# Optimization experiments

Measured on AMD Instinct MI355X. Metric: run time of the kernel, lower is better.

The kernel has to match this reference:

```python
import jax, jax.numpy as jnp
import numpy as np

N = 50000
E = 800000
IN_DIM = 256
HID_DIM = 256
OUT_DIM = 128


def _gcn(x, src, dst, W, b):
    # PyG GCNConv: h = W x; add self-loops; sym-normalized scatter-add; + bias
    h = x @ W  # [N, out]
    deg = jax.ops.segment_sum(jnp.ones_like(dst, dtype=h.dtype), dst, num_segments=N)
    dinv = jax.lax.rsqrt(jnp.maximum(deg, 1e-12))
    norm = dinv[src] * dinv[dst]  # [E+N]
    msg = h[src] * norm[:, None]  # gather + scale
    out = jax.ops.segment_sum(msg, dst, num_segments=N)  # scatter-add
    return out + b


def _with_self_loops(edge):
    loops = jnp.arange(N, dtype=edge.dtype)
    src = jnp.concatenate([edge[0], loops])
    dst = jnp.concatenate([edge[1], loops])
    return src, dst


def setup_inputs() -> dict:
    key = jax.random.key(0)
    ks = jax.random.split(key, 20)
    d = {}
    d['x'] = jax.random.normal(ks[0], (N, IN_DIM), dtype=jnp.float32)
    d['edge_ppi'] = jax.random.randint(ks[1], (2, E), 0, N, dtype=jnp.int32)
    d['edge_path'] = jax.random.randint(ks[2], (2, E), 0, N, dtype=jnp.int32)
    d['edge_go'] = jax.random.randint(ks[3], (2, E), 0, N, dtype=jnp.int32)
    i = 4
    for name in ['ppi', 'path', 'go']:
        s1 = 1.0 / np.sqrt(IN_DIM)
        s2 = 1.0 / np.sqrt(HID_DIM)
        d[f'{name}_w1'] = jax.random.uniform(ks[i], (IN_DIM, HID_DIM), jnp.float32, -s1, s1); i += 1
        d[f'{name}_b1'] = jnp.zeros((HID_DIM,), jnp.float32)
        d[f'{name}_w2'] = jax.random.uniform(ks[i], (HID_DIM, OUT_DIM), jnp.float32, -s2, s2); i += 1
        d[f'{name}_b2'] = jnp.zeros((OUT_DIM,), jnp.float32)
    sa = 1.0 / np.sqrt(OUT_DIM)
    d['attn_w'] = jax.random.uniform(ks[i], (OUT_DIM, 1), jnp.float32, -sa, sa)
    d['attn_b'] = jnp.zeros((1,), jnp.float32)
    return d


def reference(x, edge_ppi, edge_path, edge_go,
              ppi_w1, ppi_b1, ppi_w2, ppi_b2,
              path_w1, path_b1, path_w2, path_b2,
              go_w1, go_b1, go_w2, go_b2,
              attn_w, attn_b):
    feats = []
    for edge, w1, b1, w2, b2 in [
        (edge_ppi, ppi_w1, ppi_b1, ppi_w2, ppi_b2),
        (edge_path, path_w1, path_b1, path_w2, path_b2),
        (edge_go, go_w1, go_b1, go_w2, go_b2),
    ]:
        src, dst = _with_self_loops(edge)
        h = jax.nn.relu(_gcn(x, src, dst, w1, b1))
        feats.append(_gcn(h, src, dst, w2, b2))
    all_feat = jnp.stack(feats, axis=1)  # [N, 3, out]
    attn = jax.nn.softmax(all_feat @ attn_w + attn_b, axis=1)  # [N, 3, 1]
    return jnp.sum(all_feat * attn, axis=1)  # [N, out]
```

## Files before the change

kernel.cpp:

```cpp
#include <hip/hip_runtime.h>

#define NN 50000
#define NE 800000
#define BINS 98
#define CAP 12288
#define EPB 4096
#define P1B ((NE + EPB - 1) / EPB)

typedef __attribute__((ext_vector_type(8))) short short8;
typedef __attribute__((ext_vector_type(4))) float f32x4;
typedef __attribute__((ext_vector_type(8))) unsigned short ushort8v;
typedef __attribute__((ext_vector_type(4))) unsigned short ushort4v;
typedef _Float16 half8 __attribute__((ext_vector_type(8)));

__device__ __forceinline__ ushort f2bf(float f) {
    unsigned u = __float_as_uint(f);
    unsigned r = (u + 0x7fffu + ((u >> 16) & 1u)) >> 16;
    return (ushort)r;
}
__device__ __forceinline__ float bf2f(ushort h) {
    return __uint_as_float(((unsigned)h) << 16);
}
__device__ __forceinline__ ushort f2h(float f) {
    _Float16 h = (_Float16)f;
    return __builtin_bit_cast(ushort, h);
}
__device__ __forceinline__ float h2f(ushort u) {
    return (float)__builtin_bit_cast(_Float16, u);
}


__global__ __launch_bounds__(256) void k_bin(const int* __restrict__ e0,
                                             const int* __restrict__ e1,
                                             const int* __restrict__ e2,
                                             int* __restrict__ g_cur,
                                             unsigned* __restrict__ g_bins) {
    const int br = blockIdx.x / P1B;
    const int cb = blockIdx.x % P1B;
    const int* ep = (br == 0 ? e0 : br == 1 ? e1 : e2);
    const int tid = threadIdx.x;
    const int e_base = cb * EPB;

    __shared__ int s_cnt[BINS];
    __shared__ int s_start[BINS];
    __shared__ int s_cur[BINS];
    __shared__ int s_gb[BINS];
    __shared__ unsigned s_stage[EPB];

    if (tid < BINS) s_cnt[tid] = 0;
    __syncthreads();

    int4 s4[4], d4[4];
    bool valid[4];
#pragma unroll
    for (int i = 0; i < 4; ++i) {
        int idx = e_base + i * 1024 + tid * 4;
        valid[i] = (idx < NE);
        if (valid[i]) {
            s4[i] = *(const int4*)&ep[idx];
            d4[i] = *(const int4*)&ep[NE + idx];
            atomicAdd(&s_cnt[d4[i].x >> 9], 1);
            atomicAdd(&s_cnt[d4[i].y >> 9], 1);
            atomicAdd(&s_cnt[d4[i].z >> 9], 1);
            atomicAdd(&s_cnt[d4[i].w >> 9], 1);
        }
    }
    __syncthreads();
    if (tid == 0) {
        int run = 0;
        for (int b = 0; b < BINS; ++b) {
            s_start[b] = run;
            run += s_cnt[b];
        }
    }
    __syncthreads();
    if (tid < BINS) {
        s_cur[tid] = s_start[tid];
        int c = s_cnt[tid];
        int pc = (c + 15) & ~15;
        s_gb[tid] = (c > 0) ? atomicAdd(&g_cur[br * BINS + tid], pc) : 0;
    }
    __syncthreads();

#pragma unroll
    for (int i = 0; i < 4; ++i) {
        if (valid[i]) {
            int ss[4] = {s4[i].x, s4[i].y, s4[i].z, s4[i].w};
            int dd[4] = {d4[i].x, d4[i].y, d4[i].z, d4[i].w};
#pragma unroll
            for (int q = 0; q < 4; ++q) {
                int bin = dd[q] >> 9;
                int pos = atomicAdd(&s_cur[bin], 1);
                s_stage[pos] = ((unsigned)(dd[q] & 511) << 16) | (unsigned)ss[q];
            }
        }
    }
    __syncthreads();

    for (int b = 0; b < BINS; ++b) {
        int c = s_cnt[b];
        if (c == 0) continue;
        int st = s_start[b];
        int gb = s_gb[b];
        int pc = (c + 15) & ~15;
        if (gb + pc > CAP) pc = (gb < CAP) ? (CAP - gb) : 0;
        size_t obase = (size_t)(br * BINS + b) * CAP + gb;
        for (int j = tid; j < pc; j += 256)
            g_bins[obase + j] = (j < c) ? s_stage[st + j] : 0x80000000u;
    }
}


__device__ __forceinline__ int wave_incl_scan(int v, int lane) {
#pragma unroll
    for (int d = 1; d < 64; d <<= 1) {
        int u = __shfl_up(v, d);
        if (lane >= d) v += u;
    }
    return v;
}

__global__ __launch_bounds__(256) void k_build(const unsigned* __restrict__ g_bins,
                                               const int* __restrict__ g_cur,
                                               ushort* __restrict__ g_csr,
                                               int* __restrict__ seg3,
                                               int* __restrict__ cnt3,
                                               float* __restrict__ dinv3) {
    const int bid = blockIdx.x;
    const int br = bid / BINS;
    const int b2 = bid % BINS;
    const size_t base = (size_t)bid * CAP;
    const int node0 = b2 << 9;
    const int tid = threadIdx.x;

    __shared__ int s_cnt[512];
    __shared__ int s_off[512];
    __shared__ int s_wsum[4];

    s_cnt[tid] = 0;
    s_cnt[tid + 256] = 0;
    __syncthreads();

    const int total = min(g_cur[bid], CAP);
    for (int j = tid; j < total; j += 256) {
        unsigned p = g_bins[base + j];
        if (!(p & 0x80000000u)) atomicAdd(&s_cnt[(p >> 16) & 0x1FF], 1);
    }
    __syncthreads();

    const int lane = tid & 63, w = tid >> 6;
    int c0 = s_cnt[2 * tid], c1 = s_cnt[2 * tid + 1];
    int c2 = c0 + c1;
    int incl = wave_incl_scan(c2, lane);
    if (lane == 63) s_wsum[w] = incl;
    __syncthreads();
    int wpre = 0;
    for (int i = 0; i < w; ++i) wpre += s_wsum[i];
    int ex = wpre + incl - c2;
    s_off[2 * tid] = ex;
    s_off[2 * tid + 1] = ex + c0;

#pragma unroll
    for (int q = 0; q < 2; ++q) {
        int local = 2 * tid + q;
        int node = node0 + local;
        if (node < NN) {
            int g = br * NN + node;
            int c = (q == 0) ? c0 : c1;
            seg3[g] = (int)base + s_off[local];
            cnt3[g] = c;
            dinv3[g] = rsqrtf((float)(c + 1));
        }
    }
    __syncthreads();
    s_cnt[2 * tid] = s_off[2 * tid];
    s_cnt[2 * tid + 1] = s_off[2 * tid + 1];
    __syncthreads();

    for (int j = tid; j < total; j += 256) {
        unsigned p = g_bins[base + j];
        if (!(p & 0x80000000u)) {
            int loc = (p >> 16) & 0x1FF;
            int pos = atomicAdd(&s_cnt[loc], 1);
            g_csr[base + pos] = (ushort)(p & 0xFFFFu);
        }
    }
}


__global__ __launch_bounds__(256) void k_conv_x(const float* __restrict__ x,
                                                ushort* __restrict__ xp) {
    const int wid = threadIdx.x >> 6, lane = threadIdx.x & 63;
    const int row = blockIdx.x * 4 + wid;
    if (row >= NN) return;
    float4 v = *(const float4*)&x[(size_t)row * 256 + lane * 4];
    ushort4 hi, lo;
    hi.x = f2bf(v.x); lo.x = f2bf(v.x - bf2f(hi.x));
    hi.y = f2bf(v.y); lo.y = f2bf(v.y - bf2f(hi.y));
    hi.z = f2bf(v.z); lo.z = f2bf(v.z - bf2f(hi.z));
    hi.w = f2bf(v.w); lo.w = f2bf(v.w - bf2f(hi.w));
    *(ushort4*)&xp[(size_t)row * 512 + lane * 4] = hi;
    *(ushort4*)&xp[(size_t)row * 512 + 256 + lane * 4] = lo;
}

__global__ __launch_bounds__(256) void k_conv_w1(const float* __restrict__ w0,
                                                 const float* __restrict__ w1,
                                                 const float* __restrict__ w2,
                                                 ushort* __restrict__ BT1all) {
    int idx = blockIdx.x * 256 + threadIdx.x;
    int b = idx >> 16, r = idx & 65535;
    int k = r >> 8, n = r & 255;
    const float* W = (b == 0 ? w0 : b == 1 ? w1 : w2);
    float w = W[r];
    ushort hi = f2bf(w);
    ushort lo = f2bf(w - bf2f(hi));
    ushort* row = BT1all + (size_t)b * 196608 + (size_t)n * 768;
    row[k] = hi;
    row[256 + k] = hi;
    row[512 + k] = lo;
}

__global__ __launch_bounds__(256) void k_conv_w2(const float* __restrict__ w0,
                                                 const float* __restrict__ w1,
                                                 const float* __restrict__ w2,
                                                 ushort* __restrict__ BT2all) {
    int idx = blockIdx.x * 256 + threadIdx.x;
    int b = idx >> 15, r = idx & 32767;
    int k = r >> 7, n = r & 127;
    const float* W = (b == 0 ? w0 : b == 1 ? w1 : w2);
    BT2all[(size_t)b * 32768 + (size_t)n * 256 + k] = f2h(W[r]);
}


template <int BM, int BN, int N, int KK, int AK, bool HALF, bool XSWZ>
__global__ __launch_bounds__((BM / 64) * (BN / 64) * 64) void k_gemm(
    const ushort* __restrict__ A, size_t aBatch,
    const ushort* __restrict__ BTall, int btBatch,
    const float* __restrict__ dinv3, ushort* __restrict__ Call, size_t cBatch) {
    constexpr int WGN = BN / 64, NW = (BM / 64) * WGN;
    constexpr int BK = 32;
    constexpr int MT = (NN + BM - 1) / BM, NT = N / BN, GB = MT * NT;
    constexpr int NSTEP = KK / BK;
    __shared__ ushort sA[2][BM * BK];
    __shared__ ushort sB[2][BN * BK];
    int kb, bid;
    if constexpr (XSWZ) {
        int q = blockIdx.x >> 3, r = blockIdx.x & 7;
        bid = (q / 3) * 8 + r;
        kb = q % 3;
        if (bid >= GB) return;
    } else {
        kb = blockIdx.x / GB;
        bid = blockIdx.x % GB;
    }
    const ushort* Ab = A + (size_t)kb * aBatch;
    const ushort* BT = BTall + (size_t)kb * btBatch;
    const float* dinv = dinv3 + (size_t)kb * NN;
    ushort* C = Call + (size_t)kb * cBatch;
    const int t = threadIdx.x, lane = t & 63, wid = t >> 6;
    const int wm = (wid / WGN) * 64, wn = (wid % WGN) * 64;
    const int bm = (bid / NT) * BM;
    const int bn = (bid % NT) * BN;

    f32x4 zero = {0.f, 0.f, 0.f, 0.f};
    f32x4 acc[4][4];
#pragma unroll
    for (int m = 0; m < 4; ++m)
#pragma unroll
        for (int n = 0; n < 4; ++n) acc[m][n] = zero;

    constexpr int A_ISS = (BM * BK * 2) / (NW * 1024);
    constexpr int B_ISS = (BN * BK * 2) / (NW * 1024);

    auto stage = [&](int buf, int kt) {
        const int akt = (kt >= AK) ? kt - AK : kt;
#pragma unroll
        for (int i = 0; i < A_ISS; ++i) {
            int off = (wid + i * NW) << 10;
            int la = off + lane * 16;
            int row = la >> 6;
            int slot = (la >> 4) & 3;
            int scol = (slot ^ (row & 3)) << 4;
            int grow = bm + row;
            if (grow > NN - 1) grow = NN - 1;
            const char* ga = (const char*)Ab + (size_t)grow * (AK * 2) + akt * 2 + scol;
            __builtin_amdgcn_global_load_lds(
                (__attribute__((address_space(1))) const void*)ga,
                (__attribute__((address_space(3))) void*)((char*)sA[buf] + off), 16, 0, 0);
        }
#pragma unroll
        for (int i = 0; i < B_ISS; ++i) {
            int off = (wid + i * NW) << 10;
            int la = off + lane * 16;
            int row = la >> 6;
            int slot = (la >> 4) & 3;
            int scol = (slot ^ (row & 3)) << 4;
            const char* ga = (const char*)BT + (size_t)(bn + row) * (KK * 2) + kt * 2 + scol;
            __builtin_amdgcn_global_load_lds(
                (__attribute__((address_space(1))) const void*)ga,
                (__attribute__((address_space(3))) void*)((char*)sB[buf] + off), 16, 0, 0);
        }
    };

    stage(0, 0);
    __syncthreads();

    int cur = 0;
    for (int ts = 0; ts < NSTEP; ++ts) {
        if (ts + 1 < NSTEP) stage(cur ^ 1, (ts + 1) * BK);

        const int s = lane >> 4;
        const int r0 = lane & 15;
        short8 af[4], bf[4];
#pragma unroll
        for (int m = 0; m < 4; ++m) {
            int row = wm + m * 16 + r0;
            af[m] = *(const short8*)((const char*)sA[cur] + row * 64 + ((s ^ (row & 3)) << 4));
        }
#pragma unroll
        for (int n = 0; n < 4; ++n) {
            int row = wn + n * 16 + r0;
            bf[n] = *(const short8*)((const char*)sB[cur] + row * 64 + ((s ^ (row & 3)) << 4));
        }
#pragma unroll
        for (int m = 0; m < 4; ++m)
#pragma unroll
            for (int n = 0; n < 4; ++n) {
                if constexpr (HALF)
                    acc[m][n] = __builtin_amdgcn_mfma_f32_16x16x32_f16(
                        __builtin_bit_cast(half8, af[m]), __builtin_bit_cast(half8, bf[n]),
                        acc[m][n], 0, 0, 0);
                else
                    acc[m][n] = __builtin_amdgcn_mfma_f32_16x16x32_bf16(af[m], bf[n],
                                                                        acc[m][n], 0, 0, 0);
            }
        __syncthreads();
        cur ^= 1;
    }

    const int cr0 = (lane >> 4) * 4;
    const int cc = lane & 15;
#pragma unroll
    for (int m = 0; m < 4; ++m) {
#pragma unroll
        for (int r = 0; r < 4; ++r) {
            int row = bm + wm + m * 16 + cr0 + r;
            if (row < NN) {
                float dv = dinv[row];
#pragma unroll
                for (int n = 0; n < 4; ++n)
                    C[(size_t)row * N + bn + wn + n * 16 + cc] = f2h(acc[m][n][r] * dv);
            }
        }
    }
}


#define UTOT (3 * 12500)

__global__ __launch_bounds__(256) void k_agg1(const ushort* __restrict__ hs16all,
                                              const int* __restrict__ seg3,
                                              const int* __restrict__ cnt3,
                                              const ushort* __restrict__ g_csr,
                                              const float* __restrict__ dinv3,
                                              const float* __restrict__ b1a,
                                              const float* __restrict__ b1b,
                                              const float* __restrict__ b1c,
                                              ushort* __restrict__ h1all) {
    const int x = blockIdx.x & 7, j = blockIdx.x >> 3;
    const int start = (x * UTOT) >> 3;
    const int end = ((x + 1) * UTOT) >> 3;
    const int u = start + j;
    if (u >= end) return;
    const int b = u / 12500;
    const int blk = u % 12500;

    const int wid = threadIdx.x >> 6;
    const int lane = threadIdx.x & 63;
    const int node = blk * 4 + wid;
    if (node >= NN) return;
    const int half = lane >> 5, l32 = lane & 31;
    const int g = b * NN + node;
    const ushort* hs = hs16all + (size_t)b * NN * 256;
    const ushort* csr = g_csr + seg3[g];
    const int len = cnt3[g] + 1;
    const size_t colb = (size_t)l32 * 8;

    float acc[8] = {0.f, 0.f, 0.f, 0.f, 0.f, 0.f, 0.f, 0.f};
    int i = half;
    for (; i + 6 < len; i += 8) {
        int s0 = (i == 0) ? node : (int)csr[i - 1];
        int s1 = (int)csr[i + 1];
        int s2 = (int)csr[i + 3];
        int s3 = (int)csr[i + 5];
        ushort8v v0 = *(const ushort8v*)&hs[(size_t)s0 * 256 + colb];
        ushort8v v1 = *(const ushort8v*)&hs[(size_t)s1 * 256 + colb];
        ushort8v v2 = *(const ushort8v*)&hs[(size_t)s2 * 256 + colb];
        ushort8v v3 = *(const ushort8v*)&hs[(size_t)s3 * 256 + colb];
#pragma unroll
        for (int jq = 0; jq < 8; ++jq)
            acc[jq] += (h2f(v0[jq]) + h2f(v1[jq])) + (h2f(v2[jq]) + h2f(v3[jq]));
    }
    for (; i < len; i += 2) {
        int s = (i == 0) ? node : (int)csr[i - 1];
        ushort8v v = *(const ushort8v*)&hs[(size_t)s * 256 + colb];
#pragma unroll
        for (int jq = 0; jq < 8; ++jq) acc[jq] += h2f(v[jq]);
    }
#pragma unroll
    for (int jq = 0; jq < 8; ++jq) acc[jq] += __shfl_xor(acc[jq], 32);

    if (half == 0) {
        const float* bias = (b == 0 ? b1a : b == 1 ? b1b : b1c);
        const float di = dinv3[g];
        ushort8v o;
#pragma unroll
        for (int jq = 0; jq < 8; ++jq) {
            float r = fmaxf(di * acc[jq] + bias[l32 * 8 + jq], 0.f);
            o[jq] = f2h(r);
        }
        *(ushort8v*)&h1all[((size_t)b * NN + node) * 256 + colb] = o;
    }
}


__global__ __launch_bounds__(256) void k_final(const ushort* __restrict__ hs2all,
                                               const int* __restrict__ seg3,
                                               const int* __restrict__ cnt3,
                                               const ushort* __restrict__ g_csr,
                                               const float* __restrict__ dinv3,
                                               const float* __restrict__ b2a,
                                               const float* __restrict__ b2b,
                                               const float* __restrict__ b2c,
                                               const float* __restrict__ attn_w,
                                               const float* __restrict__ attn_b,
                                               float* __restrict__ out) {
    const int wid = threadIdx.x >> 6;
    const int lane = threadIdx.x & 63;
    const int node = blockIdx.x * 4 + wid;
    if (node >= NN) return;
    const int half = lane >> 5, l32 = lane & 31;
    const size_t colb = (size_t)l32 * 4;

    float f[3][4];
#pragma unroll
    for (int b = 0; b < 3; ++b) {
        const int g = b * NN + node;
        const ushort* hs = hs2all + (size_t)b * NN * 128;
        const ushort* csr = g_csr + seg3[g];
        const int len = cnt3[g] + 1;
        float acc[4] = {0.f, 0.f, 0.f, 0.f};
        int i = half;
        for (; i + 6 < len; i += 8) {
            int s0 = (i == 0) ? node : (int)csr[i - 1];
            int s1 = (int)csr[i + 1];
            int s2 = (int)csr[i + 3];
            int s3 = (int)csr[i + 5];
            ushort4v v0 = *(const ushort4v*)&hs[(size_t)s0 * 128 + colb];
            ushort4v v1 = *(const ushort4v*)&hs[(size_t)s1 * 128 + colb];
            ushort4v v2 = *(const ushort4v*)&hs[(size_t)s2 * 128 + colb];
            ushort4v v3 = *(const ushort4v*)&hs[(size_t)s3 * 128 + colb];
#pragma unroll
            for (int j = 0; j < 4; ++j)
                acc[j] += (h2f(v0[j]) + h2f(v1[j])) + (h2f(v2[j]) + h2f(v3[j]));
        }
        for (; i < len; i += 2) {
            int s = (i == 0) ? node : (int)csr[i - 1];
            ushort4v v = *(const ushort4v*)&hs[(size_t)s * 128 + colb];
#pragma unroll
            for (int j = 0; j < 4; ++j) acc[j] += h2f(v[j]);
        }
#pragma unroll
        for (int j = 0; j < 4; ++j) acc[j] += __shfl_xor(acc[j], 32);
        const float* bias = (b == 0 ? b2a : b == 1 ? b2b : b2c);
        const float di = dinv3[g];
#pragma unroll
        for (int j = 0; j < 4; ++j) f[b][j] = di * acc[j] + bias[l32 * 4 + j];
    }

    float4 w = *(const float4*)&attn_w[l32 * 4];
    float s0 = f[0][0] * w.x + f[0][1] * w.y + f[0][2] * w.z + f[0][3] * w.w;
    float s1 = f[1][0] * w.x + f[1][1] * w.y + f[1][2] * w.z + f[1][3] * w.w;
    float s2 = f[2][0] * w.x + f[2][1] * w.y + f[2][2] * w.z + f[2][3] * w.w;
#pragma unroll
    for (int m = 16; m >= 1; m >>= 1) {
        s0 += __shfl_xor(s0, m);
        s1 += __shfl_xor(s1, m);
        s2 += __shfl_xor(s2, m);
    }
    float bb = attn_b[0];
    s0 += bb; s1 += bb; s2 += bb;
    float mx = fmaxf(s0, fmaxf(s1, s2));
    float e0 = expf(s0 - mx), e1 = expf(s1 - mx), e2 = expf(s2 - mx);
    float inv = 1.f / (e0 + e1 + e2);
    e0 *= inv; e1 *= inv; e2 *= inv;

    if (half == 0) {
        float4 o;
        o.x = f[0][0] * e0 + f[1][0] * e1 + f[2][0] * e2;
        o.y = f[0][1] * e0 + f[1][1] * e1 + f[2][1] * e2;
        o.z = f[0][2] * e0 + f[1][2] * e1 + f[2][2] * e2;
        o.w = f[0][3] * e0 + f[1][3] * e1 + f[2][3] * e2;
        *(float4*)&out[(size_t)node * 128 + colb] = o;
    }
}


extern "C" void kernel_launch(void* const* d_in, const int* in_sizes, int n_in,
                              void* d_out, int out_size, void* d_ws, size_t ws_size,
                              hipStream_t stream) {
    const float* x = (const float*)d_in[0];
    const int* e0 = (const int*)d_in[1];
    const int* e1 = (const int*)d_in[2];
    const int* e2 = (const int*)d_in[3];
    const float* attn_w = (const float*)d_in[16];
    const float* attn_b = (const float*)d_in[17];

    char* ws = (char*)d_ws;
    size_t off = 0;
    auto alloc = [&](size_t bytes) -> void* {
        void* p = ws + off;
        off += (bytes + 255) & ~(size_t)255;
        return p;
    };

    int* g_cur      = (int*)alloc(3 * BINS * 4);
    int* seg3       = (int*)alloc((size_t)3 * NN * 4);
    int* cnt3       = (int*)alloc((size_t)3 * NN * 4);
    float* dinv3    = (float*)alloc((size_t)3 * NN * 4);
    ushort* g_csr   = (ushort*)alloc((size_t)3 * BINS * CAP * 2);
    ushort* xp      = (ushort*)alloc((size_t)NN * 512 * 2);
    ushort* hs2all  = xp;
    ushort* hs16all = (ushort*)alloc((size_t)3 * NN * 256 * 2);
    ushort* h1all   = (ushort*)alloc((size_t)3 * NN * 256 * 2);
    unsigned* g_bins = (unsigned*)h1all;
    ushort* BT1all  = (ushort*)alloc((size_t)3 * 256 * 768 * 2);
    ushort* BT2all  = (ushort*)alloc((size_t)3 * 128 * 256 * 2);

    const int WB = (NN + 3) / 4;

    hipMemsetAsync(g_cur, 0, 3 * BINS * 4, stream);
    k_conv_x<<<WB, 256, 0, stream>>>(x, xp);
    k_conv_w1<<<768, 256, 0, stream>>>((const float*)d_in[4], (const float*)d_in[8],
                                       (const float*)d_in[12], BT1all);
    k_conv_w2<<<384, 256, 0, stream>>>((const float*)d_in[6], (const float*)d_in[10],
                                       (const float*)d_in[14], BT2all);

    k_bin<<<3 * P1B, 256, 0, stream>>>(e0, e1, e2, g_cur, g_bins);
    k_build<<<3 * BINS, 256, 0, stream>>>(g_bins, g_cur, g_csr, seg3, cnt3, dinv3);

    k_gemm<128, 256, 256, 768, 512, false, true><<<1176, 512, 0, stream>>>(
        xp, 0, BT1all, 196608, dinv3, hs16all, (size_t)NN * 256);
    k_agg1<<<8 * ((UTOT + 7) / 8), 256, 0, stream>>>(
        hs16all, seg3, cnt3, g_csr, dinv3,
        (const float*)d_in[5], (const float*)d_in[9], (const float*)d_in[13], h1all);

    k_gemm<128, 128, 128, 256, 256, true, false><<<3 * 391, 256, 0, stream>>>(
        h1all, (size_t)NN * 256, BT2all, 32768, dinv3, hs2all, (size_t)NN * 128);

    k_final<<<WB, 256, 0, stream>>>(hs2all, seg3, cnt3, g_csr, dinv3,
                                    (const float*)d_in[7], (const float*)d_in[11],
                                    (const float*)d_in[15], attn_w, attn_b,
                                    (float*)d_out);
}
```

Baseline: 475.6 us.

## Partition sparse aggregation by column slices over node chunks; split final into feat+attn

The two aggregation kernels are restructured so that each wave owns a 32-column slice of one branch and walks a chunk of 32 consecutive nodes, gathering a single fp16 element per lane rather than a full row segment. Column groups are spread across the 8 XCD-interleaved block slots, so each XCD's L2 only has to cache a column slice of the gathered feature matrix, which is meant to improve cache reuse. The final stage is split into a per-branch aggregation that writes fp16 features to scratch, followed by a separate attention-softmax kernel. In exchange, the gathers become narrow 2-byte loads, the feature values pass through an extra fp16 round-trip, and one more launch is added.

```diff
diff --git a/kernel.cpp b/kernel.cpp
--- a/kernel.cpp
+++ b/kernel.cpp
@@ -7,10 +7,15 @@
 #define EPB 4096
 #define P1B ((NE + EPB - 1) / EPB)
 
+#define CH 1563
+#define CLS1 24
+#define T1 (CLS1 * CH)
+#define TPX1 (T1 / 8)
+#define CLS2 12
+#define T2 (CLS2 * CH)
+
 typedef __attribute__((ext_vector_type(8))) short short8;
 typedef __attribute__((ext_vector_type(4))) float f32x4;
-typedef __attribute__((ext_vector_type(8))) unsigned short ushort8v;
-typedef __attribute__((ext_vector_type(4))) unsigned short ushort4v;
 typedef _Float16 half8 __attribute__((ext_vector_type(8)));
 
 __device__ __forceinline__ ushort f2bf(float f) {
@@ -356,8 +361,6 @@
 }
 
 
-#define UTOT (3 * 12500)
-
 __global__ __launch_bounds__(256) void k_agg1(const ushort* __restrict__ hs16all,
                                               const int* __restrict__ seg3,
                                               const int* __restrict__ cnt3,
@@ -367,123 +370,127 @@
                                               const float* __restrict__ b1b,
                                               const float* __restrict__ b1c,
                                               ushort* __restrict__ h1all) {
-    const int x = blockIdx.x & 7, j = blockIdx.x >> 3;
-    const int start = (x * UTOT) >> 3;
-    const int end = ((x + 1) * UTOT) >> 3;
-    const int u = start + j;
-    if (u >= end) return;
-    const int b = u / 12500;
-    const int blk = u % 12500;
-
-    const int wid = threadIdx.x >> 6;
-    const int lane = threadIdx.x & 63;
-    const int node = blk * 4 + wid;
-    if (node >= NN) return;
+    const int x = blockIdx.x & 7, jb = blockIdx.x >> 3;
+    const int w = threadIdx.x >> 6, lane = threadIdx.x & 63;
+    const int tj = jb * 4 + w;
+    if (tj >= TPX1) return;
+    const int t = x * TPX1 + tj;
+    const int cls = t / CH, chunk = t % CH;
+    const int br = cls >> 3, cg = cls & 7;
     const int half = lane >> 5, l32 = lane & 31;
-    const int g = b * NN + node;
-    const ushort* hs = hs16all + (size_t)b * NN * 256;
-    const ushort* csr = g_csr + seg3[g];
-    const int len = cnt3[g] + 1;
-    const size_t colb = (size_t)l32 * 8;
-
-    float acc[8] = {0.f, 0.f, 0.f, 0.f, 0.f, 0.f, 0.f, 0.f};
-    int i = half;
-    for (; i + 6 < len; i += 8) {
-        int s0 = (i == 0) ? node : (int)csr[i - 1];
-        int s1 = (int)csr[i + 1];
-        int s2 = (int)csr[i + 3];
-        int s3 = (int)csr[i + 5];
-        ushort8v v0 = *(const ushort8v*)&hs[(size_t)s0 * 256 + colb];
-        ushort8v v1 = *(const ushort8v*)&hs[(size_t)s1 * 256 + colb];
-        ushort8v v2 = *(const ushort8v*)&hs[(size_t)s2 * 256 + colb];
-        ushort8v v3 = *(const ushort8v*)&hs[(size_t)s3 * 256 + colb];
-#pragma unroll
-        for (int jq = 0; jq < 8; ++jq)
-            acc[jq] += (h2f(v0[jq]) + h2f(v1[jq])) + (h2f(v2[jq]) + h2f(v3[jq]));
-    }
-    for (; i < len; i += 2) {
-        int s = (i == 0) ? node : (int)csr[i - 1];
-        ushort8v v = *(const ushort8v*)&hs[(size_t)s * 256 + colb];
-#pragma unroll
-        for (int jq = 0; jq < 8; ++jq) acc[jq] += h2f(v[jq]);
-    }
-#pragma unroll
-    for (int jq = 0; jq < 8; ++jq) acc[jq] += __shfl_xor(acc[jq], 32);
-
-    if (half == 0) {
-        const float* bias = (b == 0 ? b1a : b == 1 ? b1b : b1c);
-        const float di = dinv3[g];
-        ushort8v o;
-#pragma unroll
-        for (int jq = 0; jq < 8; ++jq) {
-            float r = fmaxf(di * acc[jq] + bias[l32 * 8 + jq], 0.f);
-            o[jq] = f2h(r);
-        }
-        *(ushort8v*)&h1all[((size_t)b * NN + node) * 256 + colb] = o;
-    }
-}
-
-
-__global__ __launch_bounds__(256) void k_final(const ushort* __restrict__ hs2all,
-                                               const int* __restrict__ seg3,
-                                               const int* __restrict__ cnt3,
-                                               const ushort* __restrict__ g_csr,
-                                               const float* __restrict__ dinv3,
-                                               const float* __restrict__ b2a,
-                                               const float* __restrict__ b2b,
-                                               const float* __restrict__ b2c,
-                                               const float* __restrict__ attn_w,
-                                               const float* __restrict__ attn_b,
-                                               float* __restrict__ out) {
-    const int wid = threadIdx.x >> 6;
-    const int lane = threadIdx.x & 63;
-    const int node = blockIdx.x * 4 + wid;
-    if (node >= NN) return;
-    const int half = lane >> 5, l32 = lane & 31;
-    const size_t colb = (size_t)l32 * 4;
-
-    float f[3][4];
-#pragma unroll
-    for (int b = 0; b < 3; ++b) {
-        const int g = b * NN + node;
-        const ushort* hs = hs2all + (size_t)b * NN * 128;
+    const int col = cg * 32 + l32;
+    const ushort* hs = hs16all + (size_t)br * NN * 256 + col;
+    const float* bias = (br == 0 ? b1a : br == 1 ? b1b : b1c);
+    const float bcol = bias[col];
+    const int n1 = min(chunk * 32 + 32, NN);
+
+    for (int node = chunk * 32; node < n1; ++node) {
+        const int g = br * NN + node;
         const ushort* csr = g_csr + seg3[g];
         const int len = cnt3[g] + 1;
-        float acc[4] = {0.f, 0.f, 0.f, 0.f};
+        float acc = 0.f;
         int i = half;
         for (; i + 6 < len; i += 8) {
             int s0 = (i == 0) ? node : (int)csr[i - 1];
             int s1 = (int)csr[i + 1];
             int s2 = (int)csr[i + 3];
             int s3 = (int)csr[i + 5];
-            ushort4v v0 = *(const ushort4v*)&hs[(size_t)s0 * 128 + colb];
-            ushort4v v1 = *(const ushort4v*)&hs[(size_t)s1 * 128 + colb];
-            ushort4v v2 = *(const ushort4v*)&hs[(size_t)s2 * 128 + colb];
-            ushort4v v3 = *(const ushort4v*)&hs[(size_t)s3 * 128 + colb];
-#pragma unroll
-            for (int j = 0; j < 4; ++j)
-                acc[j] += (h2f(v0[j]) + h2f(v1[j])) + (h2f(v2[j]) + h2f(v3[j]));
+            float v0 = h2f(hs[(size_t)s0 * 256]);
+            float v1 = h2f(hs[(size_t)s1 * 256]);
+            float v2 = h2f(hs[(size_t)s2 * 256]);
+            float v3 = h2f(hs[(size_t)s3 * 256]);
+            acc += (v0 + v1) + (v2 + v3);
         }
         for (; i < len; i += 2) {
             int s = (i == 0) ? node : (int)csr[i - 1];
-            ushort4v v = *(const ushort4v*)&hs[(size_t)s * 128 + colb];
-#pragma unroll
-            for (int j = 0; j < 4; ++j) acc[j] += h2f(v[j]);
-        }
-#pragma unroll
-        for (int j = 0; j < 4; ++j) acc[j] += __shfl_xor(acc[j], 32);
-        const float* bias = (b == 0 ? b2a : b == 1 ? b2b : b2c);
-        const float di = dinv3[g];
-#pragma unroll
-        for (int j = 0; j < 4; ++j) f[b][j] = di * acc[j] + bias[l32 * 4 + j];
-    }
-
-    float4 w = *(const float4*)&attn_w[l32 * 4];
-    float s0 = f[0][0] * w.x + f[0][1] * w.y + f[0][2] * w.z + f[0][3] * w.w;
-    float s1 = f[1][0] * w.x + f[1][1] * w.y + f[1][2] * w.z + f[1][3] * w.w;
-    float s2 = f[2][0] * w.x + f[2][1] * w.y + f[2][2] * w.z + f[2][3] * w.w;
-#pragma unroll
-    for (int m = 16; m >= 1; m >>= 1) {
+            acc += h2f(hs[(size_t)s * 256]);
+        }
+        acc += __shfl_xor(acc, 32);
+        if (half == 0) {
+            float r = fmaxf(dinv3[g] * acc + bcol, 0.f);
+            h1all[(size_t)g * 256 + col] = f2h(r);
+        }
+    }
+}
+
+
+__global__ __launch_bounds__(256) void k_feat(const ushort* __restrict__ hs2all,
+                                              const int* __restrict__ seg3,
+                                              const int* __restrict__ cnt3,
+                                              const ushort* __restrict__ g_csr,
+                                              const float* __restrict__ dinv3,
+                                              const float* __restrict__ b2a,
+                                              const float* __restrict__ b2b,
+                                              const float* __restrict__ b2c,
+                                              ushort* __restrict__ feats) {
+    const int x = blockIdx.x & 7, jb = blockIdx.x >> 3;
+    const int w = threadIdx.x >> 6, lane = threadIdx.x & 63;
+    const int start = (x * T2) >> 3;
+    const int end = ((x + 1) * T2) >> 3;
+    const int t = start + jb * 4 + w;
+    if (t >= end) return;
+    const int cls = t / CH, chunk = t % CH;
+    const int br = cls >> 2, cg = cls & 3;
+    const int half = lane >> 5, l32 = lane & 31;
+    const int col = cg * 32 + l32;
+    const ushort* hs = hs2all + (size_t)br * NN * 128 + col;
+    const float* bias = (br == 0 ? b2a : br == 1 ? b2b : b2c);
+    const float bcol = bias[col];
+    const int n1 = min(chunk * 32 + 32, NN);
+
+    for (int node = chunk * 32; node < n1; ++node) {
+        const int g = br * NN + node;
+        const ushort* csr = g_csr + seg3[g];
+        const int len = cnt3[g] + 1;
+        float acc = 0.f;
+        int i = half;
+        for (; i + 6 < len; i += 8) {
+            int s0 = (i == 0) ? node : (int)csr[i - 1];
+            int s1 = (int)csr[i + 1];
+            int s2 = (int)csr[i + 3];
+            int s3 = (int)csr[i + 5];
+            float v0 = h2f(hs[(size_t)s0 * 128]);
+            float v1 = h2f(hs[(size_t)s1 * 128]);
+            float v2 = h2f(hs[(size_t)s2 * 128]);
+            float v3 = h2f(hs[(size_t)s3 * 128]);
+            acc += (v0 + v1) + (v2 + v3);
+        }
+        for (; i < len; i += 2) {
+            int s = (i == 0) ? node : (int)csr[i - 1];
+            acc += h2f(hs[(size_t)s * 128]);
+        }
+        acc += __shfl_xor(acc, 32);
+        if (half == 0) {
+            float f = dinv3[g] * acc + bcol;
+            feats[(size_t)node * 384 + br * 128 + col] = f2h(f);
+        }
+    }
+}
+
+
+__global__ __launch_bounds__(256) void k_attn(const ushort* __restrict__ feats,
+                                              const float* __restrict__ attn_w,
+                                              const float* __restrict__ attn_b,
+                                              float* __restrict__ out) {
+    const int wid = threadIdx.x >> 6;
+    const int lane = threadIdx.x & 63;
+    const int node = blockIdx.x * 4 + wid;
+    if (node >= NN) return;
+
+    float2 w = *(const float2*)&attn_w[lane * 2];
+    const ushort* f = feats + (size_t)node * 384;
+    ushort2 u0 = *(const ushort2*)&f[0 * 128 + lane * 2];
+    ushort2 u1 = *(const ushort2*)&f[1 * 128 + lane * 2];
+    ushort2 u2 = *(const ushort2*)&f[2 * 128 + lane * 2];
+    float f0x = h2f(u0.x), f0y = h2f(u0.y);
+    float f1x = h2f(u1.x), f1y = h2f(u1.y);
+    float f2x = h2f(u2.x), f2y = h2f(u2.y);
+
+    float s0 = f0x * w.x + f0y * w.y;
+    float s1 = f1x * w.x + f1y * w.y;
+    float s2 = f2x * w.x + f2y * w.y;
+#pragma unroll
+    for (int m = 32; m >= 1; m >>= 1) {
         s0 += __shfl_xor(s0, m);
         s1 += __shfl_xor(s1, m);
         s2 += __shfl_xor(s2, m);
@@ -495,14 +502,10 @@
     float inv = 1.f / (e0 + e1 + e2);
     e0 *= inv; e1 *= inv; e2 *= inv;
 
-    if (half == 0) {
-        float4 o;
-        o.x = f[0][0] * e0 + f[1][0] * e1 + f[2][0] * e2;
-        o.y = f[0][1] * e0 + f[1][1] * e1 + f[2][1] * e2;
-        o.z = f[0][2] * e0 + f[1][2] * e1 + f[2][2] * e2;
-        o.w = f[0][3] * e0 + f[1][3] * e1 + f[2][3] * e2;
-        *(float4*)&out[(size_t)node * 128 + colb] = o;
-    }
+    float2 o;
+    o.x = f0x * e0 + f1x * e1 + f2x * e2;
+    o.y = f0y * e0 + f1y * e1 + f2y * e2;
+    *(float2*)&out[(size_t)node * 128 + lane * 2] = o;
 }
 
 
@@ -534,6 +537,7 @@
     ushort* hs16all = (ushort*)alloc((size_t)3 * NN * 256 * 2);
     ushort* h1all   = (ushort*)alloc((size_t)3 * NN * 256 * 2);
     unsigned* g_bins = (unsigned*)h1all;
+    ushort* feats   = h1all;
     ushort* BT1all  = (ushort*)alloc((size_t)3 * 256 * 768 * 2);
     ushort* BT2all  = (ushort*)alloc((size_t)3 * 128 * 256 * 2);
 
@@ -551,15 +555,15 @@
 
     k_gemm<128, 256, 256, 768, 512, false, true><<<1176, 512, 0, stream>>>(
         xp, 0, BT1all, 196608, dinv3, hs16all, (size_t)NN * 256);
-    k_agg1<<<8 * ((UTOT + 7) / 8), 256, 0, stream>>>(
+    k_agg1<<<8 * ((TPX1 + 3) / 4), 256, 0, stream>>>(
         hs16all, seg3, cnt3, g_csr, dinv3,
         (const float*)d_in[5], (const float*)d_in[9], (const float*)d_in[13], h1all);
 
     k_gemm<128, 128, 128, 256, 256, true, false><<<3 * 391, 256, 0, stream>>>(
         h1all, (size_t)NN * 256, BT2all, 32768, dinv3, hs2all, (size_t)NN * 128);
 
-    k_final<<<WB, 256, 0, stream>>>(hs2all, seg3, cnt3, g_csr, dinv3,
-                                    (const float*)d_in[7], (const float*)d_in[11],
-                                    (const float*)d_in[15], attn_w, attn_b,
-                                    (float*)d_out);
-}
+    k_feat<<<8 * ((((T2 + 7) / 8) + 3) / 4), 256, 0, stream>>>(
+        hs2all, seg3, cnt3, g_csr, dinv3,
+        (const float*)d_in[7], (const float*)d_in[11], (const float*)d_in[15], feats);
+    k_attn<<<WB, 256, 0, stream>>>(feats, attn_w, attn_b, (float*)d_out);
+}
```

New measurement: 1.028 ms. +116.1%, slower.

## Fuse layer-1 aggregation with layer-2 GEMM through shared-memory tile

Applied to the files above, without the earlier changes.

Merges the first-layer neighbor aggregation and the second-layer weight GEMM into one kernel. Each block aggregates 16 nodes into a swizzled LDS tile, then multiplies it by W2 with MFMA and writes hs2 directly. This drops the h1 intermediate round-trip to global memory and one kernel launch. In exchange, W2 is reloaded from global or L2 by every block, the output stores are narrow 2-byte writes, and the XCD-aware block remapping the old aggregation kernel used is gone.

```diff
diff --git a/kernel.cpp b/kernel.cpp
--- a/kernel.cpp
+++ b/kernel.cpp
@@ -356,70 +356,97 @@
 }
 
 
-#define UTOT (3 * 12500)
-
-__global__ __launch_bounds__(256) void k_agg1(const ushort* __restrict__ hs16all,
-                                              const int* __restrict__ seg3,
-                                              const int* __restrict__ cnt3,
-                                              const ushort* __restrict__ g_csr,
-                                              const float* __restrict__ dinv3,
-                                              const float* __restrict__ b1a,
-                                              const float* __restrict__ b1b,
-                                              const float* __restrict__ b1c,
-                                              ushort* __restrict__ h1all) {
-    const int x = blockIdx.x & 7, j = blockIdx.x >> 3;
-    const int start = (x * UTOT) >> 3;
-    const int end = ((x + 1) * UTOT) >> 3;
-    const int u = start + j;
-    if (u >= end) return;
-    const int b = u / 12500;
-    const int blk = u % 12500;
-
-    const int wid = threadIdx.x >> 6;
-    const int lane = threadIdx.x & 63;
-    const int node = blk * 4 + wid;
-    if (node >= NN) return;
+__global__ __launch_bounds__(256) void k_agg1g2(
+    const ushort* __restrict__ hs16all, const int* __restrict__ seg3,
+    const int* __restrict__ cnt3, const ushort* __restrict__ g_csr,
+    const float* __restrict__ dinv3,
+    const float* __restrict__ b1a, const float* __restrict__ b1b,
+    const float* __restrict__ b1c,
+    const ushort* __restrict__ BT2all, ushort* __restrict__ hs2all) {
+    const int br = blockIdx.x / 3125;
+    const int blk = blockIdx.x % 3125;
+    const int node0 = blk * 16;
+    const int w = threadIdx.x >> 6, lane = threadIdx.x & 63;
     const int half = lane >> 5, l32 = lane & 31;
-    const int g = b * NN + node;
-    const ushort* hs = hs16all + (size_t)b * NN * 256;
-    const ushort* csr = g_csr + seg3[g];
-    const int len = cnt3[g] + 1;
+
+    __shared__ ushort h1s[16 * 256];
+
+    const ushort* hs = hs16all + (size_t)br * NN * 256;
+    const float* bias = (br == 0 ? b1a : br == 1 ? b1b : b1c);
     const size_t colb = (size_t)l32 * 8;
 
-    float acc[8] = {0.f, 0.f, 0.f, 0.f, 0.f, 0.f, 0.f, 0.f};
-    int i = half;
-    for (; i + 6 < len; i += 8) {
-        int s0 = (i == 0) ? node : (int)csr[i - 1];
-        int s1 = (int)csr[i + 1];
-        int s2 = (int)csr[i + 3];
-        int s3 = (int)csr[i + 5];
-        ushort8v v0 = *(const ushort8v*)&hs[(size_t)s0 * 256 + colb];
-        ushort8v v1 = *(const ushort8v*)&hs[(size_t)s1 * 256 + colb];
-        ushort8v v2 = *(const ushort8v*)&hs[(size_t)s2 * 256 + colb];
-        ushort8v v3 = *(const ushort8v*)&hs[(size_t)s3 * 256 + colb];
-#pragma unroll
-        for (int jq = 0; jq < 8; ++jq)
-            acc[jq] += (h2f(v0[jq]) + h2f(v1[jq])) + (h2f(v2[jq]) + h2f(v3[jq]));
-    }
-    for (; i < len; i += 2) {
-        int s = (i == 0) ? node : (int)csr[i - 1];
-        ushort8v v = *(const ushort8v*)&hs[(size_t)s * 256 + colb];
-#pragma unroll
-        for (int jq = 0; jq < 8; ++jq) acc[jq] += h2f(v[jq]);
-    }
-#pragma unroll
-    for (int jq = 0; jq < 8; ++jq) acc[jq] += __shfl_xor(acc[jq], 32);
-
-    if (half == 0) {
-        const float* bias = (b == 0 ? b1a : b == 1 ? b1b : b1c);
-        const float di = dinv3[g];
-        ushort8v o;
-#pragma unroll
-        for (int jq = 0; jq < 8; ++jq) {
-            float r = fmaxf(di * acc[jq] + bias[l32 * 8 + jq], 0.f);
-            o[jq] = f2h(r);
-        }
-        *(ushort8v*)&h1all[((size_t)b * NN + node) * 256 + colb] = o;
+#pragma unroll 1
+    for (int q = 0; q < 4; ++q) {
+        const int r = w * 4 + q;
+        const int node = node0 + r;
+        const int g = br * NN + node;
+        const ushort* csr = g_csr + seg3[g];
+        const int len = cnt3[g] + 1;
+
+        float acc[8] = {0.f, 0.f, 0.f, 0.f, 0.f, 0.f, 0.f, 0.f};
+        int i = half;
+        for (; i + 6 < len; i += 8) {
+            int s0 = (i == 0) ? node : (int)csr[i - 1];
+            int s1 = (int)csr[i + 1];
+            int s2 = (int)csr[i + 3];
+            int s3 = (int)csr[i + 5];
+            ushort8v v0 = *(const ushort8v*)&hs[(size_t)s0 * 256 + colb];
+            ushort8v v1 = *(const ushort8v*)&hs[(size_t)s1 * 256 + colb];
+            ushort8v v2 = *(const ushort8v*)&hs[(size_t)s2 * 256 + colb];
+            ushort8v v3 = *(const ushort8v*)&hs[(size_t)s3 * 256 + colb];
+#pragma unroll
+            for (int j = 0; j < 8; ++j)
+                acc[j] += (h2f(v0[j]) + h2f(v1[j])) + (h2f(v2[j]) + h2f(v3[j]));
+        }
+        for (; i < len; i += 2) {
+            int s = (i == 0) ? node : (int)csr[i - 1];
+            ushort8v v = *(const ushort8v*)&hs[(size_t)s * 256 + colb];
+#pragma unroll
+            for (int j = 0; j < 8; ++j) acc[j] += h2f(v[j]);
+        }
+#pragma unroll
+        for (int j = 0; j < 8; ++j) acc[j] += __shfl_xor(acc[j], 32);
+
+        if (half == 0) {
+            const float di = dinv3[g];
+            ushort8v o;
+#pragma unroll
+            for (int j = 0; j < 8; ++j) {
+                float rr = fmaxf(di * acc[j] + bias[l32 * 8 + j], 0.f);
+                o[j] = f2h(rr);
+            }
+            *(ushort8v*)((char*)h1s + r * 512 + ((l32 ^ (r & 7)) << 4)) = o;
+        }
+    }
+    __syncthreads();
+
+    const int r0 = lane & 15, s = lane >> 4;
+    const int wn = w * 32;
+    const ushort* BT2 = BT2all + (size_t)br * 32768;
+    f32x4 zero = {0.f, 0.f, 0.f, 0.f};
+    f32x4 acc0 = zero, acc1 = zero;
+#pragma unroll
+    for (int ks = 0; ks < 8; ++ks) {
+        const int kt = ks * 32;
+        const int slot = ((kt >> 3) + s) ^ (r0 & 7);
+        short8 a = *(const short8*)((const char*)h1s + r0 * 512 + (slot << 4));
+        short8 b0 = *(const short8*)&BT2[(size_t)(wn + r0) * 256 + kt + s * 8];
+        short8 b1 = *(const short8*)&BT2[(size_t)(wn + 16 + r0) * 256 + kt + s * 8];
+        acc0 = __builtin_amdgcn_mfma_f32_16x16x32_f16(
+            __builtin_bit_cast(half8, a), __builtin_bit_cast(half8, b0), acc0, 0, 0, 0);
+        acc1 = __builtin_amdgcn_mfma_f32_16x16x32_f16(
+            __builtin_bit_cast(half8, a), __builtin_bit_cast(half8, b1), acc1, 0, 0, 0);
+    }
+
+    const int cc = lane & 15;
+    const int rbase = (lane >> 4) * 4;
+#pragma unroll
+    for (int rg = 0; rg < 4; ++rg) {
+        const int node = node0 + rbase + rg;
+        const float dv = dinv3[br * NN + node];
+        ushort* orow = hs2all + ((size_t)br * NN + node) * 128;
+        orow[wn + cc] = f2h(acc0[rg] * dv);
+        orow[wn + 16 + cc] = f2h(acc1[rg] * dv);
     }
 }
 
@@ -529,11 +556,10 @@
     int* cnt3       = (int*)alloc((size_t)3 * NN * 4);
     float* dinv3    = (float*)alloc((size_t)3 * NN * 4);
     ushort* g_csr   = (ushort*)alloc((size_t)3 * BINS * CAP * 2);
+    unsigned* g_bins = (unsigned*)alloc((size_t)3 * BINS * CAP * 4);
     ushort* xp      = (ushort*)alloc((size_t)NN * 512 * 2);
     ushort* hs2all  = xp;
     ushort* hs16all = (ushort*)alloc((size_t)3 * NN * 256 * 2);
-    ushort* h1all   = (ushort*)alloc((size_t)3 * NN * 256 * 2);
-    unsigned* g_bins = (unsigned*)h1all;
     ushort* BT1all  = (ushort*)alloc((size_t)3 * 256 * 768 * 2);
     ushort* BT2all  = (ushort*)alloc((size_t)3 * 128 * 256 * 2);
 
@@ -551,12 +577,11 @@
 
     k_gemm<128, 256, 256, 768, 512, false, true><<<1176, 512, 0, stream>>>(
         xp, 0, BT1all, 196608, dinv3, hs16all, (size_t)NN * 256);
-    k_agg1<<<8 * ((UTOT + 7) / 8), 256, 0, stream>>>(
+
+    k_agg1g2<<<3 * 3125, 256, 0, stream>>>(
         hs16all, seg3, cnt3, g_csr, dinv3,
-        (const float*)d_in[5], (const float*)d_in[9], (const float*)d_in[13], h1all);
-
-    k_gemm<128, 128, 128, 256, 256, true, false><<<3 * 391, 256, 0, stream>>>(
-        h1all, (size_t)NN * 256, BT2all, 32768, dinv3, hs2all, (size_t)NN * 128);
+        (const float*)d_in[5], (const float*)d_in[9], (const float*)d_in[13],
+        BT2all, hs2all);
 
     k_final<<<WB, 256, 0, stream>>>(hs2all, seg3, cnt3, g_csr, dinv3,
                                     (const float*)d_in[7], (const float*)d_in[11],
```

Result: slower. 494.8 us (+4.0%).
